# Kernel tuning notes

Hardware: AMD Instinct MI355X
Metric: run time of the kernel (lower is better)

## Reference

```python
import jax, jax.numpy as jnp
import numpy as np

N_POINTS = 1_000_000
NUM_PILLARS = 30_000
BN_EPS = 1e-3


def _bn(x, gamma, beta, mean, var):
    # eval-mode BatchNorm1d with eps=0.001
    return (x - mean) * (gamma * jax.lax.rsqrt(var + BN_EPS)) + beta


def setup_inputs() -> dict:
    key = jax.random.key(0)
    ks = jax.random.split(key, 5)
    C1, C2 = 32, 64
    return {
        "points": jax.random.normal(ks[0], (N_POINTS, 5), dtype=jnp.float32),
        "f_center": jax.random.normal(ks[1], (N_POINTS, 3), dtype=jnp.float32),
        "unq_inv": jax.random.randint(ks[2], (N_POINTS,), 0, NUM_PILLARS, dtype=jnp.int32),
        "W1": jax.random.normal(ks[3], (7, C1), dtype=jnp.float32) * 0.1,
        "g1": jnp.ones((C1,), jnp.float32),
        "b1": jnp.zeros((C1,), jnp.float32),
        "m1": jnp.zeros((C1,), jnp.float32),
        "v1": jnp.ones((C1,), jnp.float32),
        "W2": jax.random.normal(ks[4], (C2, C1), dtype=jnp.float32) * 0.1,
        "g2": jnp.ones((C1,), jnp.float32),
        "b2": jnp.zeros((C1,), jnp.float32),
        "m2": jnp.zeros((C1,), jnp.float32),
        "v2": jnp.ones((C1,), jnp.float32),
    }


def reference(points, f_center, unq_inv, W1, g1, b1, m1, v1, W2, g2, b2, m2, v2):
    # gen_feat: concat(f_center, points[:,1:]) -> Linear(no bias) -> BN -> ReLU
    feats = jnp.concatenate([f_center, points[:, 1:]], axis=-1)  # [N, 7]
    h = jnp.maximum(_bn(feats @ W1, g1, b1, m1, v1), 0.0)        # [N, 32]

    # scatter_mean over pillars, then gather back and concat
    seg_sum = jax.ops.segment_sum(h, unq_inv, num_segments=NUM_PILLARS)
    counts = jax.ops.segment_sum(jnp.ones((h.shape[0],), h.dtype), unq_inv,
                                 num_segments=NUM_PILLARS)
    seg_mean = seg_sum / jnp.maximum(counts, 1.0)[:, None]       # [P, 32]
    h2 = jnp.concatenate([h, seg_mean[unq_inv]], axis=1)         # [N, 64]

    # AVFEO: Linear(64,32,no bias) -> BN -> ReLU
    out_fc = jnp.maximum(_bn(h2 @ W2, g2, b2, m2, v2), 0.0)      # [N, 32]

    # scatter_max over pillars (empty pillars -> 0, as torch_scatter)
    seg_max = jax.ops.segment_max(out_fc, unq_inv, num_segments=NUM_PILLARS)
    return jnp.where(jnp.isfinite(seg_max), seg_max, 0.0)        # [P, 32]
```

## Files before the change

kernel.cpp:

```cpp
#include <hip/hip_runtime.h>

typedef __attribute__((ext_vector_type(8))) short short8;
typedef __attribute__((ext_vector_type(4))) float floatx4;

static constexpr float EPS = 1e-3f;

#define CAP 96
#define CSTRIDE 32

#define P_W1F  0
#define P_B1F  224
#define P_W2L  256
#define P_B2F  1280
#define P_W2UT 1312
#define PREP_F 2048

__device__ __forceinline__ unsigned short f2bf(float x) {
  unsigned u = __float_as_uint(x);
  u += 0x7FFFu + ((u >> 16) & 1u);
  return (unsigned short)(u >> 16);
}

__global__ __launch_bounds__(256)
void k_prep(const float* __restrict__ W1, const float* __restrict__ g1,
            const float* __restrict__ b1, const float* __restrict__ m1,
            const float* __restrict__ v1,
            const float* __restrict__ W2, const float* __restrict__ g2,
            const float* __restrict__ b2, const float* __restrict__ m2,
            const float* __restrict__ v2, float* __restrict__ prep) {
  int t = threadIdx.x;
  for (int i = t; i < 224; i += 256) {
    int c = i & 31;
    prep[P_W1F + i] = W1[i] * (g1[c] * rsqrtf(v1[c] + EPS));
  }
  if (t < 32) {
    float s1 = g1[t] * rsqrtf(v1[t] + EPS);
    float s2 = g2[t] * rsqrtf(v2[t] + EPS);
    prep[P_B1F + t] = b1[t] - m1[t] * s1;
    prep[P_B2F + t] = b2[t] - m2[t] * s2;
  }
  unsigned short* wt = (unsigned short*)(prep + P_W2UT);
  for (int i = t; i < 1024; i += 256) {
    int k = i >> 5, c = i & 31;
    float s2 = g2[c] * rsqrtf(v2[c] + EPS);
    prep[P_W2L + i] = W2[(32 + k) * 32 + c] * s2;
    wt[c * 32 + k] = f2bf(W2[k * 32 + c] * s2);
  }
}

__global__ __launch_bounds__(256)
void k_build_feat(const float* __restrict__ points, const float* __restrict__ fc,
                  const int* __restrict__ unq, int* __restrict__ cnt,
                  float* __restrict__ feat, int N) {
  int i = blockIdx.x * 256 + threadIdx.x;
  if (i >= N) return;
  int p = unq[i];
  float4 a, b;
  a.x = fc[3 * i];         a.y = fc[3 * i + 1];     a.z = fc[3 * i + 2];
  a.w = points[5 * i + 1];
  b.x = points[5 * i + 2]; b.y = points[5 * i + 3]; b.z = points[5 * i + 4];
  b.w = 0.f;
  int slot = atomicAdd(&cnt[p * CSTRIDE], 1);
  if (slot < CAP) {
    float4* dst = (float4*)(feat + ((size_t)p * CAP + slot) * 8);
    dst[0] = a;
    dst[1] = b;
  }
}

__global__ __launch_bounds__(256)
void k_pillar(const float* __restrict__ prep, const int* __restrict__ cnt,
              const float* __restrict__ feat, float* __restrict__ out,
              int npil) {
  __shared__ __align__(16) float fbuf[4][CAP * 8];
  __shared__ __align__(16) unsigned short hbuf[4][CAP * 32];
  __shared__ __align__(16) unsigned short w2t[1024];
  __shared__ float sumb[4][32];

  const int t = threadIdx.x, w = t >> 6, lane = t & 63;

  ((uint2*)w2t)[t] = ((const uint2*)(prep + P_W2UT))[t];
  __syncthreads();

  const int p = blockIdx.x * 4 + w;
  if (p >= npil) return;
  int n = cnt[p * CSTRIDE];
  n = n < CAP ? n : CAP;

  const int c = lane & 31, half = lane >> 5;

  const floatx4* src4 = (const floatx4*)(feat + (size_t)p * CAP * 8);
  floatx4* f4 = (floatx4*)fbuf[w];
  for (int q = lane; q < 2 * n; q += 64) f4[q] = src4[q];
  __builtin_amdgcn_wave_barrier();

  float w1c[7];
#pragma unroll
  for (int r = 0; r < 7; ++r) w1c[r] = prep[P_W1F + r * 32 + c];
  const float b1c = prep[P_B1F + c];
  const float b2c = prep[P_B2F + c];

  float ps = 0.f;
  for (int j = half; j < n; j += 2) {
    const float* f = fbuf[w] + j * 8;
    floatx4 fa = *(const floatx4*)f, fb = *(const floatx4*)(f + 4);
    float d = fa.x * w1c[0];
    d = fmaf(fa.y, w1c[1], d);
    d = fmaf(fa.z, w1c[2], d);
    d = fmaf(fa.w, w1c[3], d);
    d = fmaf(fb.x, w1c[4], d);
    d = fmaf(fb.y, w1c[5], d);
    d = fmaf(fb.z, w1c[6], d);
    float h = fmaxf(d + b1c, 0.f);
    ps += h;
    hbuf[w][j * 32 + c] = f2bf(h);
  }
  ps += __shfl_xor(ps, 32);
  if (half == 0) sumb[w][c] = ps;
  __builtin_amdgcn_wave_barrier();

  float acc = 0.f;
  const floatx4* sb4 = (const floatx4*)sumb[w];
#pragma unroll
  for (int kq = 0; kq < 8; ++kq) {
    floatx4 sv = sb4[kq];
    acc = fmaf(sv.x, prep[P_W2L + (kq * 4 + 0) * 32 + c], acc);
    acc = fmaf(sv.y, prep[P_W2L + (kq * 4 + 1) * 32 + c], acc);
    acc = fmaf(sv.z, prep[P_W2L + (kq * 4 + 2) * 32 + c], acc);
    acc = fmaf(sv.w, prep[P_W2L + (kq * 4 + 3) * 32 + c], acc);
  }
  const float inv_n = (n > 0) ? 1.f / (float)n : 1.f;
  const float pc = fmaf(inv_n, acc, b2c);

  const int m16 = lane & 15, q4 = lane >> 4;
  short8 bf0 = *(const short8*)(w2t + m16 * 32 + q4 * 8);
  short8 bf1 = *(const short8*)(w2t + (m16 + 16) * 32 + q4 * 8);
  float m0 = -INFINITY, m1 = -INFINITY;
  const int ntiles = (n + 15) >> 4;
  for (int rt = 0; rt < ntiles; ++rt) {
    short8 af = *(const short8*)(hbuf[w] + (rt * 16 + m16) * 32 + q4 * 8);
    floatx4 z = {0.f, 0.f, 0.f, 0.f};
    floatx4 a0 = __builtin_amdgcn_mfma_f32_16x16x32_bf16(af, bf0, z, 0, 0, 0);
    floatx4 a1 = __builtin_amdgcn_mfma_f32_16x16x32_bf16(af, bf1, z, 0, 0, 0);
    const int rowb = rt * 16 + q4 * 4;
#pragma unroll
    for (int r = 0; r < 4; ++r) {
      if (rowb + r < n) {
        m0 = fmaxf(m0, a0[r]);
        m1 = fmaxf(m1, a1[r]);
      }
    }
  }
  m0 = fmaxf(m0, __shfl_xor(m0, 16));
  m0 = fmaxf(m0, __shfl_xor(m0, 32));
  m1 = fmaxf(m1, __shfl_xor(m1, 16));
  m1 = fmaxf(m1, __shfl_xor(m1, 32));

  if (lane < 32) {
    float q = (lane & 16) ? m1 : m0;
    out[p * 32 + lane] = fmaxf(q + pc, 0.f);
  }
}

extern "C" void kernel_launch(void* const* d_in, const int* in_sizes, int n_in,
                              void* d_out, int out_size, void* d_ws, size_t ws_size,
                              hipStream_t stream) {
  const float* points = (const float*)d_in[0];
  const float* fc     = (const float*)d_in[1];
  const int*   unq    = (const int*)d_in[2];
  const float* W1 = (const float*)d_in[3];
  const float* g1 = (const float*)d_in[4];
  const float* b1 = (const float*)d_in[5];
  const float* m1 = (const float*)d_in[6];
  const float* v1 = (const float*)d_in[7];
  const float* W2 = (const float*)d_in[8];
  const float* g2 = (const float*)d_in[9];
  const float* b2 = (const float*)d_in[10];
  const float* m2 = (const float*)d_in[11];
  const float* v2 = (const float*)d_in[12];

  const int N    = in_sizes[0] / 5;
  const int NPIL = out_size / 32;

  float* ws = (float*)d_ws;
  int* cnt = (int*)ws;
  const size_t cnt_f  = ((size_t)NPIL * CSTRIDE + 255) & ~(size_t)255;
  float* prep = ws + cnt_f;
  float* feat = prep + PREP_F;

  hipMemsetAsync(cnt, 0, (size_t)NPIL * CSTRIDE * sizeof(int), stream);

  k_prep<<<1, 256, 0, stream>>>(W1, g1, b1, m1, v1, W2, g2, b2, m2, v2, prep);

  const int nb = (N + 255) / 256;
  k_build_feat<<<nb, 256, 0, stream>>>(points, fc, unq, cnt, feat, N);

  const int nbp = (NPIL + 3) / 4;
  k_pillar<<<nbp, 256, 0, stream>>>(prep, cnt, feat, (float*)d_out, NPIL);
}
```

Before: 186.6 us.

## Bucket point indices instead of features, gather inputs inside pillar kernel

The bucketing kernel now writes only a 4-byte point index per slot instead of a 32-byte packed feature record. The pillar kernel reads those indices and gathers f_center and points directly from the original arrays into shared memory. This cuts scattered global writes and the later re-read of the feature buffer. In exchange the per-pillar loads become random gathers with unaligned vector accesses.

```diff
diff --git a/kernel.cpp b/kernel.cpp
--- a/kernel.cpp
+++ b/kernel.cpp
@@ -2,6 +2,8 @@
 
 typedef __attribute__((ext_vector_type(8))) short short8;
 typedef __attribute__((ext_vector_type(4))) float floatx4;
+typedef __attribute__((ext_vector_type(2), aligned(4))) float f2a;
+typedef __attribute__((ext_vector_type(4), aligned(4))) float f4a;
 
 static constexpr float EPS = 1e-3f;
 
@@ -49,28 +51,19 @@
 }
 
 __global__ __launch_bounds__(256)
-void k_build_feat(const float* __restrict__ points, const float* __restrict__ fc,
-                  const int* __restrict__ unq, int* __restrict__ cnt,
-                  float* __restrict__ feat, int N) {
+void k_build_idx(const int* __restrict__ unq, int* __restrict__ cnt,
+                 int* __restrict__ idx, int N) {
   int i = blockIdx.x * 256 + threadIdx.x;
   if (i >= N) return;
   int p = unq[i];
-  float4 a, b;
-  a.x = fc[3 * i];         a.y = fc[3 * i + 1];     a.z = fc[3 * i + 2];
-  a.w = points[5 * i + 1];
-  b.x = points[5 * i + 2]; b.y = points[5 * i + 3]; b.z = points[5 * i + 4];
-  b.w = 0.f;
   int slot = atomicAdd(&cnt[p * CSTRIDE], 1);
-  if (slot < CAP) {
-    float4* dst = (float4*)(feat + ((size_t)p * CAP + slot) * 8);
-    dst[0] = a;
-    dst[1] = b;
-  }
+  if (slot < CAP) idx[p * CAP + slot] = i;
 }
 
 __global__ __launch_bounds__(256)
 void k_pillar(const float* __restrict__ prep, const int* __restrict__ cnt,
-              const float* __restrict__ feat, float* __restrict__ out,
+              const int* __restrict__ idx, const float* __restrict__ points,
+              const float* __restrict__ fc, float* __restrict__ out,
               int npil) {
   __shared__ __align__(16) float fbuf[4][CAP * 8];
   __shared__ __align__(16) unsigned short hbuf[4][CAP * 32];
@@ -89,9 +82,19 @@
 
   const int c = lane & 31, half = lane >> 5;
 
-  const floatx4* src4 = (const floatx4*)(feat + (size_t)p * CAP * 8);
-  floatx4* f4 = (floatx4*)fbuf[w];
-  for (int q = lane; q < 2 * n; q += 64) f4[q] = src4[q];
+  const int* idxp = idx + (size_t)p * CAP;
+  for (int q = lane; q < n; q += 64) {
+    int i = idxp[q];
+    f2a c2 = *(const f2a*)(fc + 3 * (size_t)i);
+    float cz = fc[3 * (size_t)i + 2];
+    f4a p4 = *(const f4a*)(points + 5 * (size_t)i + 1);
+    floatx4 A, B;
+    A.x = c2.x; A.y = c2.y; A.z = cz;  A.w = p4.x;
+    B.x = p4.y; B.y = p4.z; B.z = p4.w; B.w = 0.f;
+    floatx4* d4 = (floatx4*)(fbuf[w] + q * 8);
+    d4[0] = A;
+    d4[1] = B;
+  }
   __builtin_amdgcn_wave_barrier();
 
   float w1c[7];
@@ -186,15 +189,15 @@
   int* cnt = (int*)ws;
   const size_t cnt_f  = ((size_t)NPIL * CSTRIDE + 255) & ~(size_t)255;
   float* prep = ws + cnt_f;
-  float* feat = prep + PREP_F;
+  int* idx = (int*)(prep + PREP_F);
 
   hipMemsetAsync(cnt, 0, (size_t)NPIL * CSTRIDE * sizeof(int), stream);
 
   k_prep<<<1, 256, 0, stream>>>(W1, g1, b1, m1, v1, W2, g2, b2, m2, v2, prep);
 
   const int nb = (N + 255) / 256;
-  k_build_feat<<<nb, 256, 0, stream>>>(points, fc, unq, cnt, feat, N);
+  k_build_idx<<<nb, 256, 0, stream>>>(unq, cnt, idx, N);
 
   const int nbp = (NPIL + 3) / 4;
-  k_pillar<<<nbp, 256, 0, stream>>>(prep, cnt, feat, (float*)d_out, NPIL);
-}
+  k_pillar<<<nbp, 256, 0, stream>>>(prep, cnt, idx, points, fc, (float*)d_out, NPIL);
+}
```

Measured after the change: 218.2 us. +16.9%, slower.

## Compute first layer in the scatter kernel and store fp16 activations per pillar

Applied to the files above, without the earlier changes.

The weight-prep kernel is folded into the point-scatter kernel. That kernel now stages the point inputs in LDS through coalesced nontemporal loads, computes the 7→32 linear+BN+ReLU per point, and scatters 32 fp16 activations into per-pillar slots. The pillar kernel then only copies the fp16 rows, sums them, and runs the second GEMM with f16 MFMA instead of bf16. This removes the per-pillar layer-1 recomputation and one launch. In exchange, the bytes written and read per point double (64 B instead of 32 B), and the slot capacity now comes from the workspace size, capped at 80, so overflowing pillars would silently drop points.

```diff
diff --git a/kernel.cpp b/kernel.cpp
--- a/kernel.cpp
+++ b/kernel.cpp
@@ -1,79 +1,108 @@
 #include <hip/hip_runtime.h>
 
 typedef __attribute__((ext_vector_type(8))) short short8;
+typedef __attribute__((ext_vector_type(8))) _Float16 half8;
 typedef __attribute__((ext_vector_type(4))) float floatx4;
+typedef __attribute__((ext_vector_type(4))) unsigned int uintx4;
 
 static constexpr float EPS = 1e-3f;
 
-#define CAP 96
 #define CSTRIDE 32
-
-#define P_W1F  0
-#define P_B1F  224
-#define P_W2L  256
-#define P_B2F  1280
-#define P_W2UT 1312
+#define CAPMAX 80
+
+#define P_W2L  0
+#define P_B2F  1024
+#define P_W2UT 1056
 #define PREP_F 2048
 
-__device__ __forceinline__ unsigned short f2bf(float x) {
-  unsigned u = __float_as_uint(x);
-  u += 0x7FFFu + ((u >> 16) & 1u);
-  return (unsigned short)(u >> 16);
-}
-
 __global__ __launch_bounds__(256)
-void k_prep(const float* __restrict__ W1, const float* __restrict__ g1,
-            const float* __restrict__ b1, const float* __restrict__ m1,
-            const float* __restrict__ v1,
-            const float* __restrict__ W2, const float* __restrict__ g2,
-            const float* __restrict__ b2, const float* __restrict__ m2,
-            const float* __restrict__ v2, float* __restrict__ prep) {
-  int t = threadIdx.x;
-  for (int i = t; i < 224; i += 256) {
-    int c = i & 31;
-    prep[P_W1F + i] = W1[i] * (g1[c] * rsqrtf(v1[c] + EPS));
+void k_build(const float* __restrict__ points, const float* __restrict__ fc,
+             const int* __restrict__ unq, int* __restrict__ cnt,
+             unsigned short* __restrict__ hreg,
+             const float* __restrict__ W1, const float* __restrict__ g1,
+             const float* __restrict__ b1, const float* __restrict__ m1,
+             const float* __restrict__ v1,
+             const float* __restrict__ W2, const float* __restrict__ g2,
+             const float* __restrict__ b2, const float* __restrict__ m2,
+             const float* __restrict__ v2, float* __restrict__ prep,
+             int N, int caph) {
+  __shared__ float w1f[224];
+  __shared__ float b1f[32];
+  __shared__ float lfc[256 * 3];
+  __shared__ float lpt[256 * 5];
+  __shared__ int   sbase[256];
+
+  const int t = threadIdx.x;
+  const int ibase = blockIdx.x * 256;
+  const int nloc = min(256, N - ibase);
+
+  if (blockIdx.x == 0) {
+    if (t < 32) {
+      float s2 = g2[t] * rsqrtf(v2[t] + EPS);
+      prep[P_B2F + t] = b2[t] - m2[t] * s2;
+    }
+    _Float16* wt = (_Float16*)(prep + P_W2UT);
+    for (int i2 = t; i2 < 1024; i2 += 256) {
+      int k = i2 >> 5, c = i2 & 31;
+      float s2 = g2[c] * rsqrtf(v2[c] + EPS);
+      prep[P_W2L + i2] = W2[(32 + k) * 32 + c] * s2;
+      wt[c * 32 + k] = (_Float16)(W2[k * 32 + c] * s2);
+    }
+  }
+
+  if (t < 224) {
+    int c = t & 31;
+    w1f[t] = W1[t] * (g1[c] * rsqrtf(v1[c] + EPS));
   }
   if (t < 32) {
     float s1 = g1[t] * rsqrtf(v1[t] + EPS);
-    float s2 = g2[t] * rsqrtf(v2[t] + EPS);
-    prep[P_B1F + t] = b1[t] - m1[t] * s1;
-    prep[P_B2F + t] = b2[t] - m2[t] * s2;
-  }
-  unsigned short* wt = (unsigned short*)(prep + P_W2UT);
-  for (int i = t; i < 1024; i += 256) {
-    int k = i >> 5, c = i & 31;
-    float s2 = g2[c] * rsqrtf(v2[c] + EPS);
-    prep[P_W2L + i] = W2[(32 + k) * 32 + c] * s2;
-    wt[c * 32 + k] = f2bf(W2[k * 32 + c] * s2);
-  }
-}
-
-__global__ __launch_bounds__(256)
-void k_build_feat(const float* __restrict__ points, const float* __restrict__ fc,
-                  const int* __restrict__ unq, int* __restrict__ cnt,
-                  float* __restrict__ feat, int N) {
-  int i = blockIdx.x * 256 + threadIdx.x;
-  if (i >= N) return;
-  int p = unq[i];
-  float4 a, b;
-  a.x = fc[3 * i];         a.y = fc[3 * i + 1];     a.z = fc[3 * i + 2];
-  a.w = points[5 * i + 1];
-  b.x = points[5 * i + 2]; b.y = points[5 * i + 3]; b.z = points[5 * i + 4];
-  b.w = 0.f;
-  int slot = atomicAdd(&cnt[p * CSTRIDE], 1);
-  if (slot < CAP) {
-    float4* dst = (float4*)(feat + ((size_t)p * CAP + slot) * 8);
-    dst[0] = a;
-    dst[1] = b;
+    b1f[t] = b1[t] - m1[t] * s1;
+  }
+
+  for (int k = t; k < nloc * 3; k += 256)
+    lfc[k] = __builtin_nontemporal_load(fc + (size_t)ibase * 3 + k);
+  for (int k = t; k < nloc * 5; k += 256)
+    lpt[k] = __builtin_nontemporal_load(points + (size_t)ibase * 5 + k);
+
+  if (t < nloc) {
+    int p = __builtin_nontemporal_load(unq + ibase + t);
+    int slot = atomicAdd(&cnt[p * CSTRIDE], 1);
+    sbase[t] = (slot < caph) ? (p * caph + slot) : -1;
+  } else {
+    sbase[t] = -1;
+  }
+
+  __syncthreads();
+
+  const int hw = t >> 5, c = t & 31;
+  float w1c[7];
+#pragma unroll
+  for (int r = 0; r < 7; ++r) w1c[r] = w1f[r * 32 + c];
+  const float b1c = b1f[c];
+
+  for (int jj = 0; jj < 32; ++jj) {
+    const int j = hw * 32 + jj;
+    const int sb = sbase[j];
+    float d = lfc[3 * j] * w1c[0];
+    d = fmaf(lfc[3 * j + 1], w1c[1], d);
+    d = fmaf(lfc[3 * j + 2], w1c[2], d);
+    d = fmaf(lpt[5 * j + 1], w1c[3], d);
+    d = fmaf(lpt[5 * j + 2], w1c[4], d);
+    d = fmaf(lpt[5 * j + 3], w1c[5], d);
+    d = fmaf(lpt[5 * j + 4], w1c[6], d);
+    float h = fmaxf(d + b1c, 0.f);
+    _Float16 hh = (_Float16)h;
+    if (sb >= 0)
+      __builtin_nontemporal_store(__builtin_bit_cast(unsigned short, hh),
+                                  hreg + (size_t)sb * 32 + c);
   }
 }
 
 __global__ __launch_bounds__(256)
 void k_pillar(const float* __restrict__ prep, const int* __restrict__ cnt,
-              const float* __restrict__ feat, float* __restrict__ out,
-              int npil) {
-  __shared__ __align__(16) float fbuf[4][CAP * 8];
-  __shared__ __align__(16) unsigned short hbuf[4][CAP * 32];
+              const unsigned short* __restrict__ hreg, float* __restrict__ out,
+              int npil, int caph) {
+  __shared__ __align__(16) unsigned short hbuf[4][CAPMAX * 32];
   __shared__ __align__(16) unsigned short w2t[1024];
   __shared__ float sumb[4][32];
 
@@ -85,36 +114,28 @@
   const int p = blockIdx.x * 4 + w;
   if (p >= npil) return;
   int n = cnt[p * CSTRIDE];
-  n = n < CAP ? n : CAP;
+  n = n < caph ? n : caph;
+
+  {
+    const unsigned short* src = hreg + (size_t)p * caph * 32;
+    const int jr = lane >> 2, ch = lane & 3;
+    for (int base = 0; base < n; base += 16) {
+      int j = base + jr;
+      if (j < n) {
+        uintx4 v = __builtin_nontemporal_load(
+            (const uintx4*)(src + j * 32 + ch * 8));
+        *(uintx4*)&hbuf[w][j * 32 + ch * 8] = v;
+      }
+    }
+  }
+  __builtin_amdgcn_wave_barrier();
 
   const int c = lane & 31, half = lane >> 5;
-
-  const floatx4* src4 = (const floatx4*)(feat + (size_t)p * CAP * 8);
-  floatx4* f4 = (floatx4*)fbuf[w];
-  for (int q = lane; q < 2 * n; q += 64) f4[q] = src4[q];
-  __builtin_amdgcn_wave_barrier();
-
-  float w1c[7];
-#pragma unroll
-  for (int r = 0; r < 7; ++r) w1c[r] = prep[P_W1F + r * 32 + c];
-  const float b1c = prep[P_B1F + c];
   const float b2c = prep[P_B2F + c];
 
   float ps = 0.f;
-  for (int j = half; j < n; j += 2) {
-    const float* f = fbuf[w] + j * 8;
-    floatx4 fa = *(const floatx4*)f, fb = *(const floatx4*)(f + 4);
-    float d = fa.x * w1c[0];
-    d = fmaf(fa.y, w1c[1], d);
-    d = fmaf(fa.z, w1c[2], d);
-    d = fmaf(fa.w, w1c[3], d);
-    d = fmaf(fb.x, w1c[4], d);
-    d = fmaf(fb.y, w1c[5], d);
-    d = fmaf(fb.z, w1c[6], d);
-    float h = fmaxf(d + b1c, 0.f);
-    ps += h;
-    hbuf[w][j * 32 + c] = f2bf(h);
-  }
+  const _Float16* hb = (const _Float16*)hbuf[w];
+  for (int j = half; j < n; j += 2) ps += (float)hb[j * 32 + c];
   ps += __shfl_xor(ps, 32);
   if (half == 0) sumb[w][c] = ps;
   __builtin_amdgcn_wave_barrier();
@@ -133,15 +154,15 @@
   const float pc = fmaf(inv_n, acc, b2c);
 
   const int m16 = lane & 15, q4 = lane >> 4;
-  short8 bf0 = *(const short8*)(w2t + m16 * 32 + q4 * 8);
-  short8 bf1 = *(const short8*)(w2t + (m16 + 16) * 32 + q4 * 8);
+  half8 bf0 = *(const half8*)(w2t + m16 * 32 + q4 * 8);
+  half8 bf1 = *(const half8*)(w2t + (m16 + 16) * 32 + q4 * 8);
   float m0 = -INFINITY, m1 = -INFINITY;
   const int ntiles = (n + 15) >> 4;
   for (int rt = 0; rt < ntiles; ++rt) {
-    short8 af = *(const short8*)(hbuf[w] + (rt * 16 + m16) * 32 + q4 * 8);
+    half8 af = *(const half8*)(hbuf[w] + (rt * 16 + m16) * 32 + q4 * 8);
     floatx4 z = {0.f, 0.f, 0.f, 0.f};
-    floatx4 a0 = __builtin_amdgcn_mfma_f32_16x16x32_bf16(af, bf0, z, 0, 0, 0);
-    floatx4 a1 = __builtin_amdgcn_mfma_f32_16x16x32_bf16(af, bf1, z, 0, 0, 0);
+    floatx4 a0 = __builtin_amdgcn_mfma_f32_16x16x32_f16(af, bf0, z, 0, 0, 0);
+    floatx4 a1 = __builtin_amdgcn_mfma_f32_16x16x32_f16(af, bf1, z, 0, 0, 0);
     const int rowb = rt * 16 + q4 * 4;
 #pragma unroll
     for (int r = 0; r < 4; ++r) {
@@ -184,17 +205,22 @@
 
   float* ws = (float*)d_ws;
   int* cnt = (int*)ws;
-  const size_t cnt_f  = ((size_t)NPIL * CSTRIDE + 255) & ~(size_t)255;
+  const size_t cnt_f = ((size_t)NPIL * CSTRIDE + 255) & ~(size_t)255;
   float* prep = ws + cnt_f;
-  float* feat = prep + PREP_F;
+  unsigned short* hreg = (unsigned short*)(prep + PREP_F);
+
+  const size_t hreg_halves = (ws_size / 4 - cnt_f - PREP_F) * 2;
+  int caph = (int)(hreg_halves / (32 * (size_t)NPIL));
+  if (caph > CAPMAX) caph = CAPMAX;
+  if (caph < 1) caph = 1;
 
   hipMemsetAsync(cnt, 0, (size_t)NPIL * CSTRIDE * sizeof(int), stream);
 
-  k_prep<<<1, 256, 0, stream>>>(W1, g1, b1, m1, v1, W2, g2, b2, m2, v2, prep);
-
   const int nb = (N + 255) / 256;
-  k_build_feat<<<nb, 256, 0, stream>>>(points, fc, unq, cnt, feat, N);
+  k_build<<<nb, 256, 0, stream>>>(points, fc, unq, cnt, hreg,
+                                  W1, g1, b1, m1, v1,
+                                  W2, g2, b2, m2, v2, prep, N, caph);
 
   const int nbp = (NPIL + 3) / 4;
-  k_pillar<<<nbp, 256, 0, stream>>>(prep, cnt, feat, (float*)d_out, NPIL);
+  k_pillar<<<nbp, 256, 0, stream>>>(prep, cnt, hreg, (float*)d_out, NPIL, caph);
 }
```

New measurement: 198.7 us. 6.5% more time.
